# Performance work log

Hardware: AMD Instinct MI355X
Metric: run time of the kernel (lower is better)

The kernel has to match this reference:

```python
import jax, jax.numpy as jnp
import numpy as np

H, D, Kd, Vd = 16, 1024, 64, 64
N, Mlen = 4096, 4096


def setup_inputs() -> dict:
    key = jax.random.key(0)
    ks = jax.random.split(key, 7)
    X = jax.random.normal(ks[0], (N, D), dtype=jnp.float32)
    M = jax.random.normal(ks[1], (Mlen, D), dtype=jnp.float32)
    mask = jax.random.randint(ks[2], (N, Mlen), 0, 2, dtype=jnp.int32)
    Wq = jax.random.normal(ks[3], (H, D, Kd), dtype=jnp.float32)
    Wk = jax.random.normal(ks[4], (H, D, Kd), dtype=jnp.float32)
    Wv = jax.random.normal(ks[5], (H, D, Vd), dtype=jnp.float32)
    Wo = jax.random.normal(ks[6], (H, Vd, D), dtype=jnp.float32)
    return {"X": X, "M": M, "mask": mask, "Wq": Wq, "Wk": Wk, "Wv": Wv, "Wo": Wo}


def reference(X, M, mask, Wq, Wk, Wv, Wo):
    # Projections: [h,n,k], [h,m,k], [h,m,v]
    Q = jnp.einsum('nd,hdk->hnk', X, Wq)
    K = jnp.einsum('md,hdk->hmk', M, Wk)
    V = jnp.einsum('md,hdv->hmv', M, Wv)
    # Masked attention (no scaling, matching the source)
    logits = jnp.einsum('hnk,hmk->hnm', Q, K)
    logits = jnp.where(mask[None, :, :] == 0, -jnp.inf, logits)
    weights = jax.nn.softmax(logits, axis=-1)
    O = jnp.einsum('hnm,hmv->hnv', weights, V)
    Y = jnp.einsum('hnv,hvd->nd', O, Wo)
    return Y
```

## Files before the change

### kernel.cpp

```cpp
#include <hip/hip_runtime.h>

typedef _Float16 half8 __attribute__((ext_vector_type(8)));
typedef _Float16 half2v __attribute__((ext_vector_type(2)));
typedef short short8 __attribute__((ext_vector_type(8)));
typedef short short4v __attribute__((ext_vector_type(4)));
typedef float floatx4 __attribute__((ext_vector_type(4)));

#define GLDS16(g, l) __builtin_amdgcn_global_load_lds( \
    (const __attribute__((address_space(1))) unsigned int*)(g), \
    (__attribute__((address_space(3))) unsigned int*)(l), 16, 0, 0)

static __device__ __forceinline__ short f2bf(float f){
  union { float f; unsigned u; } v; v.f = f;
  unsigned r = v.u + 0x7fffu + ((v.u >> 16) & 1u);
  return (short)(r >> 16);
}
static __device__ __forceinline__ float bf2f(short s){
  union { unsigned u; float f; } v; v.u = ((unsigned)(unsigned short)s) << 16;
  return v.f;
}

__global__ __launch_bounds__(256) void kconvA(const float* __restrict__ X,
                                              const float* __restrict__ Mm,
                                              short* __restrict__ XFh, short* __restrict__ XFl,
                                              short* __restrict__ MFh, short* __restrict__ MFl){
  int b = blockIdx.x;
  int t = threadIdx.x, w = t >> 6, l = t & 63, quad = l >> 4;
  int srcsel = b >> 8, ntile = b & 255;
  const float* A = srcsel ? Mm : X;
  short* oh = srcsel ? MFh : XFh;
  short* ol = srcsel ? MFl : XFl;
  int row = ntile*16 + (l & 15);
  #pragma unroll
  for (int i = 0; i < 8; i++){
    int kt = w*8 + i;
    const float* p = A + (size_t)row*1024 + kt*32 + quad*8;
    float4 v0 = *(const float4*)p, v1 = *(const float4*)(p + 4);
    float vv[8] = {v0.x,v0.y,v0.z,v0.w,v1.x,v1.y,v1.z,v1.w};
    short8 hh, ll;
    #pragma unroll
    for (int j = 0; j < 8; j++){
      short hb = f2bf(vv[j]); hh[j] = hb; ll[j] = f2bf(vv[j] - bf2f(hb));
    }
    size_t off = ((size_t)kt*256 + ntile)*512 + l*8;
    *(short8*)&oh[off] = hh;
    *(short8*)&ol[off] = ll;
  }
}

__global__ __launch_bounds__(256) void kconvW2(const float* __restrict__ Wq,
                                               const float* __restrict__ Wk,
                                               const float* __restrict__ Wv,
                                               short* __restrict__ WFh, short* __restrict__ WFl){
  __shared__ float T[128][68];
  int bidx = blockIdx.x, g = blockIdx.y;
  int mat = bidx >> 4, h = bidx & 15;
  const float* W = (mat == 0 ? Wq : (mat == 1 ? Wk : Wv)) + (size_t)h*65536;
  int t = threadIdx.x, w = t >> 6, l = t & 63, quad = (l >> 4) & 3, fl = l & 15;
  #pragma unroll
  for (int p = 0; p < 32; p++){
    int idx = p*256 + t, row = idx >> 6, col = idx & 63;
    T[row][col] = W[(size_t)(g*128 + row)*64 + col];
  }
  __syncthreads();
  for (int ktl = 0; ktl < 4; ktl++){
    short8 hh, ll;
    #pragma unroll
    for (int j = 0; j < 8; j++){
      float v = T[ktl*32 + quad*8 + j][w*16 + fl];
      short hb = f2bf(v); hh[j] = hb; ll[j] = f2bf(v - bf2f(hb));
    }
    size_t frag = ((size_t)bidx*32 + g*4 + ktl)*4 + w;
    *(short8*)&WFh[frag*512 + l*8] = hh;
    *(short8*)&WFl[frag*512 + l*8] = ll;
  }
}

__global__ __launch_bounds__(256) void kmaskpack(const int* __restrict__ mask,
                                                 unsigned* __restrict__ bits){
  int w = blockIdx.x * 256 + threadIdx.x;
  const int* p = mask + (size_t)w * 32;
  unsigned b = 0;
  #pragma unroll
  for (int i = 0; i < 32; i++) b |= (p[i] != 0) ? (1u << i) : 0u;
  bits[w] = b;
}

__global__ __launch_bounds__(256) void ktransw(const float* __restrict__ src,
                                               short* __restrict__ dsth,
                                               short* __restrict__ dstl,
                                               int R, int C){
  __shared__ float tile[32][33];
  size_t boff = (size_t)blockIdx.z * R * C;
  src += boff; dsth += boff; dstl += boff;
  int r0 = blockIdx.y*32, c0 = blockIdx.x*32;
  int t = threadIdx.x, tr = t >> 3, tc = (t & 7)*4;
  const float* s = src + (size_t)(r0 + tr)*C + c0 + tc;
  #pragma unroll
  for (int i = 0; i < 4; i++) tile[tr][tc + i] = s[i];
  __syncthreads();
  short* dh = dsth + (size_t)(c0 + tr)*R + r0 + tc;
  short* dl = dstl + (size_t)(c0 + tr)*R + r0 + tc;
  #pragma unroll
  for (int i = 0; i < 4; i++){
    float v = tile[tc + i][tr];
    short hb = f2bf(v);
    dh[i] = hb; dl[i] = f2bf(v - bf2f(hb));
  }
}

__global__ __launch_bounds__(256,2) void kproj2(
    const short* __restrict__ XFh, const short* __restrict__ XFl,
    const short* __restrict__ MFh, const short* __restrict__ MFl,
    const short* __restrict__ WFh, const short* __restrict__ WFl,
    _Float16* __restrict__ QFh, _Float16* __restrict__ QFl,
    _Float16* __restrict__ KFh, _Float16* __restrict__ KFl,
    _Float16* __restrict__ VF)
{
  __shared__ short AhL[4096], AlL[4096], BhL[2048], BlL[2048];
  int cb = blockIdx.x, rb = blockIdx.y;
  int mat = cb >> 4, h = cb & 15;
  const short* Ah = (mat == 0) ? XFh : MFh;
  const short* Al = (mat == 0) ? XFl : MFl;
  int t = threadIdx.x, w = t >> 6, l = t & 63, quad = l >> 4, ln = l & 15;
  floatx4 acc[2][4] = {};
  for (int kt = 0; kt < 32; kt++){
    __syncthreads();
    size_t abase = ((size_t)kt*256 + rb*8)*512;
    #pragma unroll
    for (int i = 0; i < 2; i++){
      int cidx = i*256 + t;
      GLDS16(Ah + abase + cidx*8, &AhL[(i*256 + w*64)*8]);
      GLDS16(Al + abase + cidx*8, &AlL[(i*256 + w*64)*8]);
    }
    size_t bbase = (((size_t)cb*32 + kt)*4)*512;
    GLDS16(WFh + bbase + t*8, &BhL[(w*64)*8]);
    GLDS16(WFl + bbase + t*8, &BlL[(w*64)*8]);
    __syncthreads();
    short8 bh[4], bl[4];
    #pragma unroll
    for (int nt = 0; nt < 4; nt++){
      bh[nt] = *(short8*)&BhL[nt*512 + l*8];
      bl[nt] = *(short8*)&BlL[nt*512 + l*8];
    }
    #pragma unroll
    for (int mt = 0; mt < 2; mt++){
      short8 ah = *(short8*)&AhL[(w*2 + mt)*512 + l*8];
      short8 al = *(short8*)&AlL[(w*2 + mt)*512 + l*8];
      #pragma unroll
      for (int nt = 0; nt < 4; nt++){
        acc[mt][nt] = __builtin_amdgcn_mfma_f32_16x16x32_bf16(ah, bh[nt], acc[mt][nt], 0, 0, 0);
        acc[mt][nt] = __builtin_amdgcn_mfma_f32_16x16x32_bf16(ah, bl[nt], acc[mt][nt], 0, 0, 0);
        acc[mt][nt] = __builtin_amdgcn_mfma_f32_16x16x32_bf16(al, bh[nt], acc[mt][nt], 0, 0, 0);
      }
    }
  }
  int row0 = rb*128;
  #pragma unroll
  for (int mt = 0; mt < 2; mt++)
    #pragma unroll
    for (int nt = 0; nt < 4; nt++)
      #pragma unroll
      for (int rg = 0; rg < 4; rg++){
        int n = row0 + w*32 + mt*16 + quad*4 + rg;
        int c = nt*16 + ln;
        float v = acc[mt][nt][rg];
        if (mat == 2){
          int lane2 = ln + (((n >> 3) & 3) << 4);
          VF[(((size_t)h*128 + (n >> 5))*4 + nt)*512 + lane2*8 + (n & 7)] = (_Float16)v;
        } else {
          _Float16 hi = (_Float16)v;
          _Float16 lo = (_Float16)(v - (float)hi);
          int lane2 = (n & 15) + (((c >> 3) & 3) << 4);
          size_t off = (((size_t)h*256 + (n >> 4))*2 + (c >> 5))*512 + lane2*8 + (c & 7);
          if (mat == 0){ QFh[off] = hi; QFl[off] = lo; }
          else         { KFh[off] = hi; KFl[off] = lo; }
        }
      }
}

__global__ __launch_bounds__(256,3) void kattn3(
    const _Float16* __restrict__ QFh, const _Float16* __restrict__ QFl,
    const _Float16* __restrict__ KFh, const _Float16* __restrict__ KFl,
    const _Float16* __restrict__ VF, const unsigned* __restrict__ bits,
    short* __restrict__ Ows)
{
  __shared__ _Float16 KBh[8192], KBl[8192], VB[8192];
  __shared__ _Float16 Pscr[4][16][40];
  int bx = blockIdx.x, h = bx & 15, qb = bx >> 4, q0 = qb*128;
  int t = threadIdx.x, w = t >> 6, l = t & 63, quad = l >> 4, ln = l & 15;

  half8 qh[2][2], ql[2][2];
  #pragma unroll
  for (int nt2 = 0; nt2 < 2; nt2++)
    #pragma unroll
    for (int kc = 0; kc < 2; kc++){
      size_t off = (((size_t)h*256 + qb*8 + w*2 + nt2)*2 + kc)*512 + l*8;
      qh[nt2][kc] = *(const half8*)&QFh[off];
      ql[nt2][kc] = *(const half8*)&QFl[off];
    }

  floatx4 o[2][4] = {};
  float mst[2] = {-1e30f, -1e30f}, lst[2] = {0.f, 0.f};

  for (int kt = 0; kt < 32; kt++){
    __syncthreads();
    size_t kb = (size_t)h*262144 + (size_t)kt*8192;
    #pragma unroll
    for (int i = 0; i < 4; i++){
      int cidx = i*256 + t;
      GLDS16(KFh + kb + cidx*8, &KBh[(i*256 + w*64)*8]);
      GLDS16(KFl + kb + cidx*8, &KBl[(i*256 + w*64)*8]);
      GLDS16(VF  + kb + cidx*8, &VB [(i*256 + w*64)*8]);
    }
    uint4 mw[2];
    mw[0] = *(const uint4*)&bits[(size_t)(q0 + w*32 + ln)*128 + kt*4];
    mw[1] = *(const uint4*)&bits[(size_t)(q0 + w*32 + 16 + ln)*128 + kt*4];
    __syncthreads();

    floatx4 st[2][8] = {};
    #pragma unroll
    for (int kc = 0; kc < 2; kc++)
      #pragma unroll
      for (int m8 = 0; m8 < 8; m8++){
        half8 kh = *(half8*)&KBh[(m8*2 + kc)*512 + l*8];
        half8 kl = *(half8*)&KBl[(m8*2 + kc)*512 + l*8];
        #pragma unroll
        for (int nt2 = 0; nt2 < 2; nt2++){
          st[nt2][m8] = __builtin_amdgcn_mfma_f32_16x16x32_f16(kh, qh[nt2][kc], st[nt2][m8], 0, 0, 0);
          st[nt2][m8] = __builtin_amdgcn_mfma_f32_16x16x32_f16(kl, qh[nt2][kc], st[nt2][m8], 0, 0, 0);
          st[nt2][m8] = __builtin_amdgcn_mfma_f32_16x16x32_f16(kh, ql[nt2][kc], st[nt2][m8], 0, 0, 0);
        }
      }

    #pragma unroll
    for (int nt2 = 0; nt2 < 2; nt2++){
      const unsigned* mwp = (const unsigned*)&mw[nt2];
      #pragma unroll
      for (int m8 = 0; m8 < 8; m8++){
        unsigned nib = mwp[m8 >> 1] >> ((m8 & 1)*16 + quad*4);
        #pragma unroll
        for (int rg = 0; rg < 4; rg++)
          if (!((nib >> rg) & 1u)) st[nt2][m8][rg] = -1e30f;
      }
      float mx = st[nt2][0][0];
      #pragma unroll
      for (int m8 = 0; m8 < 8; m8++)
        #pragma unroll
        for (int rg = 0; rg < 4; rg++) mx = fmaxf(mx, st[nt2][m8][rg]);
      mx = fmaxf(mx, __shfl_xor(mx, 16));
      mx = fmaxf(mx, __shfl_xor(mx, 32));
      float mnew = fmaxf(mst[nt2], mx);
      float alpha = __expf(mst[nt2] - mnew);
      mst[nt2] = mnew;
      lst[nt2] *= alpha;
      #pragma unroll
      for (int vt = 0; vt < 4; vt++) o[nt2][vt] *= alpha;
      float s = 0.f;
      #pragma unroll
      for (int m8 = 0; m8 < 8; m8++)
        #pragma unroll
        for (int rg = 0; rg < 4; rg++){
          float p = __expf(st[nt2][m8][rg] - mnew);
          st[nt2][m8][rg] = p; s += p;
        }
      s += __shfl_xor(s, 16);
      s += __shfl_xor(s, 32);
      lst[nt2] += s;

      #pragma unroll
      for (int c = 0; c < 4; c++){
        #pragma unroll
        for (int tt = 0; tt < 2; tt++){
          int m8 = c*2 + tt;
          half2v p01, p23;
          p01[0] = (_Float16)st[nt2][m8][0]; p01[1] = (_Float16)st[nt2][m8][1];
          p23[0] = (_Float16)st[nt2][m8][2]; p23[1] = (_Float16)st[nt2][m8][3];
          *(half2v*)&Pscr[w][ln][tt*16 + quad*4]     = p01;
          *(half2v*)&Pscr[w][ln][tt*16 + quad*4 + 2] = p23;
        }
        half8 pf = *(half8*)&Pscr[w][ln][quad*8];
        #pragma unroll
        for (int vt = 0; vt < 4; vt++){
          half8 vf = *(half8*)&VB[(c*4 + vt)*512 + l*8];
          o[nt2][vt] = __builtin_amdgcn_mfma_f32_16x16x32_f16(vf, pf, o[nt2][vt], 0, 0, 0);
        }
      }
    }
  }

  #pragma unroll
  for (int nt2 = 0; nt2 < 2; nt2++){
    float inv = (lst[nt2] > 0.f) ? (1.f / lst[nt2]) : 0.f;
    int n = q0 + w*32 + nt2*16 + ln;
    #pragma unroll
    for (int vt = 0; vt < 4; vt++){
      short4v pk;
      #pragma unroll
      for (int rg = 0; rg < 4; rg++) pk[rg] = f2bf(o[nt2][vt][rg]*inv);
      *(short4v*)&Ows[(size_t)n*1024 + h*64 + vt*16 + quad*4] = pk;
    }
  }
}

__global__ __launch_bounds__(256,2) void kfinal(const short* __restrict__ Ain,
                                                const short* __restrict__ Bt,
                                                float* __restrict__ Y)
{
  __shared__ short Al[128*48];
  __shared__ short Bl[64*48];
  int cb = blockIdx.x, rb = blockIdx.y;
  int row0 = rb*128, col0 = cb*64;
  int t = threadIdx.x, w = t >> 6, l = t & 63, quad = l >> 4, ln = l & 15;
  floatx4 acc[2][4] = {};
  for (int d0 = 0; d0 < 1024; d0 += 32){
    #pragma unroll
    for (int i = 0; i < 2; i++){
      int u = t + i*256, r = u >> 2, s = u & 3;
      *(int4*)&Al[r*48 + s*8] = *(const int4*)&Ain[(size_t)(row0 + r)*1024 + d0 + s*8];
    }
    { int r = t >> 2, s = t & 3;
      *(int4*)&Bl[r*48 + s*8] = *(const int4*)&Bt[(size_t)(col0 + r)*1024 + d0 + s*8]; }
    __syncthreads();
    short8 bf[4];
    #pragma unroll
    for (int nt = 0; nt < 4; nt++) bf[nt] = *(short8*)&Bl[(nt*16 + ln)*48 + quad*8];
    #pragma unroll
    for (int mt = 0; mt < 2; mt++){
      short8 af = *(short8*)&Al[(w*32 + mt*16 + ln)*48 + quad*8];
      #pragma unroll
      for (int nt = 0; nt < 4; nt++)
        acc[mt][nt] = __builtin_amdgcn_mfma_f32_16x16x32_bf16(af, bf[nt], acc[mt][nt], 0, 0, 0);
    }
    __syncthreads();
  }
  #pragma unroll
  for (int mt = 0; mt < 2; mt++)
    #pragma unroll
    for (int nt = 0; nt < 4; nt++)
      #pragma unroll
      for (int rg = 0; rg < 4; rg++){
        int n = row0 + w*32 + mt*16 + quad*4 + rg;
        int c = col0 + nt*16 + ln;
        Y[(size_t)n*1024 + c] = acc[mt][nt][rg];
      }
}

extern "C" void kernel_launch(void* const* d_in, const int* in_sizes, int n_in,
                              void* d_out, int out_size, void* d_ws, size_t ws_size,
                              hipStream_t stream){
  (void)in_sizes; (void)n_in; (void)out_size; (void)ws_size;
  const float* X    = (const float*)d_in[0];
  const float* Mm   = (const float*)d_in[1];
  const int*   mask = (const int*)d_in[2];
  const float* Wq   = (const float*)d_in[3];
  const float* Wk   = (const float*)d_in[4];
  const float* Wv   = (const float*)d_in[5];
  const float* Wo   = (const float*)d_in[6];
  float* Y = (float*)d_out;
  char* ws = (char*)d_ws;
  const size_t MB = 1024*1024;
  short*    XFh   = (short*)   (ws +  0*MB);
  short*    XFl   = (short*)   (ws +  8*MB);
  short*    MFh   = (short*)   (ws + 16*MB);
  short*    MFl   = (short*)   (ws + 24*MB);
  short*    WFh   = (short*)   (ws + 32*MB);
  short*    WFl   = (short*)   (ws + 38*MB);
  unsigned* bits  = (unsigned*)(ws + 44*MB);
  _Float16* QFh   = (_Float16*)(ws + 46*MB);
  _Float16* QFl   = (_Float16*)(ws + 54*MB);
  _Float16* KFh   = (_Float16*)(ws + 62*MB);
  _Float16* KFl   = (_Float16*)(ws + 70*MB);
  _Float16* VF    = (_Float16*)(ws + 78*MB);
  short*    Ows   = (short*)   (ws +  0*MB);
  short*    Wot   = (short*)   (ws +  8*MB);
  short*    Wotl  = (short*)   (ws + 10*MB);

  kconvA<<<512, 256, 0, stream>>>(X, Mm, XFh, XFl, MFh, MFl);
  kconvW2<<<dim3(48,8), 256, 0, stream>>>(Wq, Wk, Wv, WFh, WFl);
  kmaskpack<<<2048, 256, 0, stream>>>(mask, bits);
  kproj2<<<dim3(48,32), 256, 0, stream>>>(XFh, XFl, MFh, MFl, WFh, WFl,
                                          QFh, QFl, KFh, KFl, VF);
  ktransw<<<dim3(32,32,1), 256, 0, stream>>>(Wo, Wot, Wotl, 1024, 1024);
  kattn3<<<512, 256, 0, stream>>>(QFh, QFl, KFh, KFl, VF, bits, Ows);
  kfinal<<<dim3(16,32), 256, 0, stream>>>(Ows, Wot, Y);
}
```

Before: 486.6 us.

## Split attention over two key halves with a combine kernel, and use exp2 softmax

```diff
diff --git a/kernel.cpp b/kernel.cpp
--- a/kernel.cpp
+++ b/kernel.cpp
@@ -1,10 +1,12 @@
 #include <hip/hip_runtime.h>
 
 typedef _Float16 half8 __attribute__((ext_vector_type(8)));
-typedef _Float16 half2v __attribute__((ext_vector_type(2)));
+typedef __fp16 fp16x2 __attribute__((ext_vector_type(2)));
 typedef short short8 __attribute__((ext_vector_type(8)));
 typedef short short4v __attribute__((ext_vector_type(4)));
 typedef float floatx4 __attribute__((ext_vector_type(4)));
+
+#define LOG2E 1.4426950408889634f
 
 #define GLDS16(g, l) __builtin_amdgcn_global_load_lds( \
     (const __attribute__((address_space(1))) unsigned int*)(g), \
@@ -169,6 +171,7 @@
           int lane2 = ln + (((n >> 3) & 3) << 4);
           VF[(((size_t)h*128 + (n >> 5))*4 + nt)*512 + lane2*8 + (n & 7)] = (_Float16)v;
         } else {
+          if (mat == 0) v *= LOG2E;
           _Float16 hi = (_Float16)v;
           _Float16 lo = (_Float16)(v - (float)hi);
           int lane2 = (n & 15) + (((c >> 3) & 3) << 4);
@@ -179,16 +182,24 @@
       }
 }
 
-__global__ __launch_bounds__(256,3) void kattn3(
+__global__ __launch_bounds__(256,3) void kattn4(
     const _Float16* __restrict__ QFh, const _Float16* __restrict__ QFl,
     const _Float16* __restrict__ KFh, const _Float16* __restrict__ KFl,
     const _Float16* __restrict__ VF, const unsigned* __restrict__ bits,
-    short* __restrict__ Ows)
+    float* __restrict__ OP, float2* __restrict__ ML)
 {
   __shared__ _Float16 KBh[8192], KBl[8192], VB[8192];
-  __shared__ _Float16 Pscr[4][16][40];
-  int bx = blockIdx.x, h = bx & 15, qb = bx >> 4, q0 = qb*128;
+  __shared__ _Float16 Pscr[4][16][36];
+  __shared__ float MLUT[16][4];
+  int bx = blockIdx.x, h = bx & 15, qb = (bx >> 4) & 31, s = bx >> 9;
+  int hq = bx & 511, q0 = qb*128;
   int t = threadIdx.x, w = t >> 6, l = t & 63, quad = l >> 4, ln = l & 15;
+
+  if (t < 16){
+    #pragma unroll
+    for (int rg = 0; rg < 4; rg++)
+      MLUT[t][rg] = ((t >> rg) & 1) ? 1e30f : -1e30f;
+  }
 
   half8 qh[2][2], ql[2][2];
   #pragma unroll
@@ -203,7 +214,7 @@
   floatx4 o[2][4] = {};
   float mst[2] = {-1e30f, -1e30f}, lst[2] = {0.f, 0.f};
 
-  for (int kt = 0; kt < 32; kt++){
+  for (int kt = s*16; kt < s*16 + 16; kt++){
     __syncthreads();
     size_t kb = (size_t)h*262144 + (size_t)kt*8192;
     #pragma unroll
@@ -238,10 +249,11 @@
       const unsigned* mwp = (const unsigned*)&mw[nt2];
       #pragma unroll
       for (int m8 = 0; m8 < 8; m8++){
-        unsigned nib = mwp[m8 >> 1] >> ((m8 & 1)*16 + quad*4);
+        unsigned nib = (mwp[m8 >> 1] >> ((m8 & 1)*16 + quad*4)) & 15u;
+        floatx4 lv = *(floatx4*)&MLUT[nib][0];
         #pragma unroll
         for (int rg = 0; rg < 4; rg++)
-          if (!((nib >> rg) & 1u)) st[nt2][m8][rg] = -1e30f;
+          st[nt2][m8][rg] = fminf(st[nt2][m8][rg], lv[rg]);
       }
       float mx = st[nt2][0][0];
       #pragma unroll
@@ -251,33 +263,32 @@
       mx = fmaxf(mx, __shfl_xor(mx, 16));
       mx = fmaxf(mx, __shfl_xor(mx, 32));
       float mnew = fmaxf(mst[nt2], mx);
-      float alpha = __expf(mst[nt2] - mnew);
+      float alpha = exp2f(mst[nt2] - mnew);
       mst[nt2] = mnew;
       lst[nt2] *= alpha;
       #pragma unroll
       for (int vt = 0; vt < 4; vt++) o[nt2][vt] *= alpha;
-      float s = 0.f;
+      float ssum = 0.f;
       #pragma unroll
       for (int m8 = 0; m8 < 8; m8++)
         #pragma unroll
         for (int rg = 0; rg < 4; rg++){
-          float p = __expf(st[nt2][m8][rg] - mnew);
-          st[nt2][m8][rg] = p; s += p;
+          float p = exp2f(st[nt2][m8][rg] - mnew);
+          st[nt2][m8][rg] = p; ssum += p;
         }
-      s += __shfl_xor(s, 16);
-      s += __shfl_xor(s, 32);
-      lst[nt2] += s;
+      ssum += __shfl_xor(ssum, 16);
+      ssum += __shfl_xor(ssum, 32);
+      lst[nt2] += ssum;
 
       #pragma unroll
       for (int c = 0; c < 4; c++){
         #pragma unroll
         for (int tt = 0; tt < 2; tt++){
           int m8 = c*2 + tt;
-          half2v p01, p23;
-          p01[0] = (_Float16)st[nt2][m8][0]; p01[1] = (_Float16)st[nt2][m8][1];
-          p23[0] = (_Float16)st[nt2][m8][2]; p23[1] = (_Float16)st[nt2][m8][3];
-          *(half2v*)&Pscr[w][ln][tt*16 + quad*4]     = p01;
-          *(half2v*)&Pscr[w][ln][tt*16 + quad*4 + 2] = p23;
+          fp16x2 p01 = __builtin_amdgcn_cvt_pkrtz(st[nt2][m8][0], st[nt2][m8][1]);
+          fp16x2 p23 = __builtin_amdgcn_cvt_pkrtz(st[nt2][m8][2], st[nt2][m8][3]);
+          *(fp16x2*)&Pscr[w][ln][tt*16 + quad*4]     = p01;
+          *(fp16x2*)&Pscr[w][ln][tt*16 + quad*4 + 2] = p23;
         }
         half8 pf = *(half8*)&Pscr[w][ln][quad*8];
         #pragma unroll
@@ -291,15 +302,41 @@
 
   #pragma unroll
   for (int nt2 = 0; nt2 < 2; nt2++){
-    float inv = (lst[nt2] > 0.f) ? (1.f / lst[nt2]) : 0.f;
-    int n = q0 + w*32 + nt2*16 + ln;
-    #pragma unroll
-    for (int vt = 0; vt < 4; vt++){
-      short4v pk;
-      #pragma unroll
-      for (int rg = 0; rg < 4; rg++) pk[rg] = f2bf(o[nt2][vt][rg]*inv);
-      *(short4v*)&Ows[(size_t)n*1024 + h*64 + vt*16 + quad*4] = pk;
-    }
+    int ql2 = w*32 + nt2*16 + ln;
+    size_t pb = (((size_t)hq*2 + s)*128 + ql2)*64;
+    #pragma unroll
+    for (int vt = 0; vt < 4; vt++)
+      *(floatx4*)&OP[pb + vt*16 + quad*4] = o[nt2][vt];
+    if (quad == 0){
+      float2 m2; m2.x = mst[nt2]; m2.y = lst[nt2];
+      ML[((size_t)hq*2 + s)*128 + ql2] = m2;
+    }
+  }
+}
+
+__global__ __launch_bounds__(256) void kcomb(const float* __restrict__ OP,
+                                             const float2* __restrict__ ML,
+                                             short* __restrict__ Ows){
+  int hq = blockIdx.x, h = hq & 15, qb = hq >> 4;
+  int t = threadIdx.x;
+  #pragma unroll
+  for (int i = 0; i < 8; i++){
+    int idx = i*256 + t;
+    int q = idx >> 4, vg = idx & 15;
+    float2 a = ML[((size_t)hq*2 + 0)*128 + q];
+    float2 b = ML[((size_t)hq*2 + 1)*128 + q];
+    float m = fmaxf(a.x, b.x);
+    float w0 = exp2f(a.x - m), w1 = exp2f(b.x - m);
+    float lsum = w0*a.y + w1*b.y;
+    float inv = (lsum > 0.f) ? (1.f / lsum) : 0.f;
+    const float* p0 = &OP[(((size_t)hq*2 + 0)*128 + q)*64 + vg*4];
+    const float* p1 = &OP[(((size_t)hq*2 + 1)*128 + q)*64 + vg*4];
+    short4v pk;
+    #pragma unroll
+    for (int rg = 0; rg < 4; rg++)
+      pk[rg] = f2bf((w0*p0[rg] + w1*p1[rg])*inv);
+    int n = qb*128 + q;
+    *(short4v*)&Ows[(size_t)n*1024 + h*64 + vg*4] = pk;
   }
 }
 
@@ -375,6 +412,8 @@
   short*    Ows   = (short*)   (ws +  0*MB);
   short*    Wot   = (short*)   (ws +  8*MB);
   short*    Wotl  = (short*)   (ws + 10*MB);
+  float*    OP    = (float*)   (ws + 12*MB);
+  float2*   ML    = (float2*)  (ws + 86*MB);
 
   kconvA<<<512, 256, 0, stream>>>(X, Mm, XFh, XFl, MFh, MFl);
   kconvW2<<<dim3(48,8), 256, 0, stream>>>(Wq, Wk, Wv, WFh, WFl);
@@ -382,6 +421,7 @@
   kproj2<<<dim3(48,32), 256, 0, stream>>>(XFh, XFl, MFh, MFl, WFh, WFl,
                                           QFh, QFl, KFh, KFl, VF);
   ktransw<<<dim3(32,32,1), 256, 0, stream>>>(Wo, Wot, Wotl, 1024, 1024);
-  kattn3<<<512, 256, 0, stream>>>(QFh, QFl, KFh, KFl, VF, bits, Ows);
+  kattn4<<<1024, 256, 0, stream>>>(QFh, QFl, KFh, KFl, VF, bits, OP, ML);
+  kcomb<<<512, 256, 0, stream>>>(OP, ML, Ows);
   kfinal<<<dim3(16,32), 256, 0, stream>>>(Ows, Wot, Y);
 }
```

After: 547.7 us. +12.5%, slower.

## Feed softmax probabilities to PV MFMA directly from registers, drop LDS scratch

Applied to the files above, without the earlier changes.

```diff
diff --git a/kernel.cpp b/kernel.cpp
--- a/kernel.cpp
+++ b/kernel.cpp
@@ -1,10 +1,13 @@
 #include <hip/hip_runtime.h>
 
 typedef _Float16 half8 __attribute__((ext_vector_type(8)));
-typedef _Float16 half2v __attribute__((ext_vector_type(2)));
+typedef _Float16 half4 __attribute__((ext_vector_type(4)));
+typedef __fp16 fp16x2 __attribute__((ext_vector_type(2)));
 typedef short short8 __attribute__((ext_vector_type(8)));
 typedef short short4v __attribute__((ext_vector_type(4)));
 typedef float floatx4 __attribute__((ext_vector_type(4)));
+
+#define LOG2E 1.4426950408889634f
 
 #define GLDS16(g, l) __builtin_amdgcn_global_load_lds( \
     (const __attribute__((address_space(1))) unsigned int*)(g), \
@@ -156,19 +159,28 @@
     }
   }
   int row0 = rb*128;
-  #pragma unroll
-  for (int mt = 0; mt < 2; mt++)
-    #pragma unroll
-    for (int nt = 0; nt < 4; nt++)
-      #pragma unroll
-      for (int rg = 0; rg < 4; rg++){
-        int n = row0 + w*32 + mt*16 + quad*4 + rg;
-        int c = nt*16 + ln;
-        float v = acc[mt][nt][rg];
-        if (mat == 2){
-          int lane2 = ln + (((n >> 3) & 3) << 4);
-          VF[(((size_t)h*128 + (n >> 5))*4 + nt)*512 + lane2*8 + (n & 7)] = (_Float16)v;
-        } else {
+  if (mat == 2){
+    #pragma unroll
+    for (int mt = 0; mt < 2; mt++)
+      #pragma unroll
+      for (int nt = 0; nt < 4; nt++){
+        union { fp16x2 h2[2]; unsigned u2[2]; } pu;
+        pu.h2[0] = __builtin_amdgcn_cvt_pkrtz(acc[mt][nt][0], acc[mt][nt][1]);
+        pu.h2[1] = __builtin_amdgcn_cvt_pkrtz(acc[mt][nt][2], acc[mt][nt][3]);
+        size_t base = (((size_t)h*32 + rb)*16 + nt*4 + w)*512;
+        *(uint2*)&VF[base + (quad*16 + ln)*8 + mt*4] = *(uint2*)&pu.u2[0];
+      }
+  } else {
+    #pragma unroll
+    for (int mt = 0; mt < 2; mt++)
+      #pragma unroll
+      for (int nt = 0; nt < 4; nt++)
+        #pragma unroll
+        for (int rg = 0; rg < 4; rg++){
+          int n = row0 + w*32 + mt*16 + quad*4 + rg;
+          int c = nt*16 + ln;
+          float v = acc[mt][nt][rg];
+          if (mat == 0) v *= LOG2E;
           _Float16 hi = (_Float16)v;
           _Float16 lo = (_Float16)(v - (float)hi);
           int lane2 = (n & 15) + (((c >> 3) & 3) << 4);
@@ -176,17 +188,16 @@
           if (mat == 0){ QFh[off] = hi; QFl[off] = lo; }
           else         { KFh[off] = hi; KFl[off] = lo; }
         }
-      }
-}
-
-__global__ __launch_bounds__(256,3) void kattn3(
+  }
+}
+
+__global__ __launch_bounds__(256,3) void kattn5(
     const _Float16* __restrict__ QFh, const _Float16* __restrict__ QFl,
     const _Float16* __restrict__ KFh, const _Float16* __restrict__ KFl,
     const _Float16* __restrict__ VF, const unsigned* __restrict__ bits,
     short* __restrict__ Ows)
 {
   __shared__ _Float16 KBh[8192], KBl[8192], VB[8192];
-  __shared__ _Float16 Pscr[4][16][40];
   int bx = blockIdx.x, h = bx & 15, qb = bx >> 4, q0 = qb*128;
   int t = threadIdx.x, w = t >> 6, l = t & 63, quad = l >> 4, ln = l & 15;
 
@@ -238,7 +249,7 @@
       const unsigned* mwp = (const unsigned*)&mw[nt2];
       #pragma unroll
       for (int m8 = 0; m8 < 8; m8++){
-        unsigned nib = mwp[m8 >> 1] >> ((m8 & 1)*16 + quad*4);
+        unsigned nib = (mwp[m8 >> 1] >> ((m8 & 1)*16 + quad*4)) & 15u;
         #pragma unroll
         for (int rg = 0; rg < 4; rg++)
           if (!((nib >> rg) & 1u)) st[nt2][m8][rg] = -1e30f;
@@ -251,47 +262,52 @@
       mx = fmaxf(mx, __shfl_xor(mx, 16));
       mx = fmaxf(mx, __shfl_xor(mx, 32));
       float mnew = fmaxf(mst[nt2], mx);
-      float alpha = __expf(mst[nt2] - mnew);
+      float alpha = exp2f(mst[nt2] - mnew);
       mst[nt2] = mnew;
       lst[nt2] *= alpha;
       #pragma unroll
       for (int vt = 0; vt < 4; vt++) o[nt2][vt] *= alpha;
-      float s = 0.f;
+      float ssum = 0.f;
       #pragma unroll
       for (int m8 = 0; m8 < 8; m8++)
         #pragma unroll
         for (int rg = 0; rg < 4; rg++){
-          float p = __expf(st[nt2][m8][rg] - mnew);
-          st[nt2][m8][rg] = p; s += p;
+          float p = exp2f(st[nt2][m8][rg] - mnew);
+          st[nt2][m8][rg] = p; ssum += p;
         }
-      s += __shfl_xor(s, 16);
-      s += __shfl_xor(s, 32);
-      lst[nt2] += s;
-
-      #pragma unroll
-      for (int c = 0; c < 4; c++){
-        #pragma unroll
-        for (int tt = 0; tt < 2; tt++){
-          int m8 = c*2 + tt;
-          half2v p01, p23;
-          p01[0] = (_Float16)st[nt2][m8][0]; p01[1] = (_Float16)st[nt2][m8][1];
-          p23[0] = (_Float16)st[nt2][m8][2]; p23[1] = (_Float16)st[nt2][m8][3];
-          *(half2v*)&Pscr[w][ln][tt*16 + quad*4]     = p01;
-          *(half2v*)&Pscr[w][ln][tt*16 + quad*4 + 2] = p23;
+      ssum += __shfl_xor(ssum, 16);
+      ssum += __shfl_xor(ssum, 32);
+      lst[nt2] += ssum;
+    }
+
+    #pragma unroll
+    for (int p = 0; p < 4; p++){
+      half8 vfp[4];
+      #pragma unroll
+      for (int vt = 0; vt < 4; vt++)
+        vfp[vt] = *(half8*)&VB[(vt*4 + p)*512 + l*8];
+      #pragma unroll
+      for (int nt2 = 0; nt2 < 2; nt2++)
+        #pragma unroll
+        for (int sub = 0; sub < 2; sub++){
+          int m8 = p*2 + sub;
+          union { fp16x2 h2[2]; half4 h4; } pu;
+          pu.h2[0] = __builtin_amdgcn_cvt_pkrtz(st[nt2][m8][0], st[nt2][m8][1]);
+          pu.h2[1] = __builtin_amdgcn_cvt_pkrtz(st[nt2][m8][2], st[nt2][m8][3]);
+          #pragma unroll
+          for (int vt = 0; vt < 4; vt++){
+            half4 va = sub ? __builtin_shufflevector(vfp[vt], vfp[vt], 4,5,6,7)
+                           : __builtin_shufflevector(vfp[vt], vfp[vt], 0,1,2,3);
+            o[nt2][vt] = __builtin_amdgcn_mfma_f32_16x16x16f16(va, pu.h4, o[nt2][vt], 0, 0, 0);
+          }
         }
-        half8 pf = *(half8*)&Pscr[w][ln][quad*8];
-        #pragma unroll
-        for (int vt = 0; vt < 4; vt++){
-          half8 vf = *(half8*)&VB[(c*4 + vt)*512 + l*8];
-          o[nt2][vt] = __builtin_amdgcn_mfma_f32_16x16x32_f16(vf, pf, o[nt2][vt], 0, 0, 0);
-        }
-      }
     }
   }
 
   #pragma unroll
   for (int nt2 = 0; nt2 < 2; nt2++){
-    float inv = (lst[nt2] > 0.f) ? (1.f / lst[nt2]) : 0.f;
+    float li = lst[nt2];
+    float inv = (li > 0.f) ? (1.f / li) : 0.f;
     int n = q0 + w*32 + nt2*16 + ln;
     #pragma unroll
     for (int vt = 0; vt < 4; vt++){
@@ -382,6 +398,6 @@
   kproj2<<<dim3(48,32), 256, 0, stream>>>(XFh, XFl, MFh, MFl, WFh, WFl,
                                           QFh, QFl, KFh, KFl, VF);
   ktransw<<<dim3(32,32,1), 256, 0, stream>>>(Wo, Wot, Wotl, 1024, 1024);
-  kattn3<<<512, 256, 0, stream>>>(QFh, QFl, KFh, KFl, VF, bits, Ows);
+  kattn5<<<512, 256, 0, stream>>>(QFh, QFl, KFh, KFl, VF, bits, Ows);
   kfinal<<<dim3(16,32), 256, 0, stream>>>(Ows, Wot, Y);
 }
```

Measured after the change: 468.1 us. 1.04x faster.
